# Optimization experiments

Hardware: AMD Instinct MI355X
Metric: run time of the kernel (lower is better)

The kernel has to match this reference:

```python
import jax, jax.numpy as jnp
import numpy as np

B, S, D = 1, 2048, 4096
NH, NKV, HD = 32, 8, 128
N_REP = NH // NKV
NEG = -1e9


def setup_inputs() -> dict:
    key = jax.random.key(0)
    ks = jax.random.split(key, 8)
    x = jax.random.normal(ks[0], (B, S, D), dtype=jnp.float32)
    # rotary freqs (theta=10000), shape [S, HD//2]
    inv = 1.0 / (10000.0 ** (jnp.arange(0, HD, 2, dtype=jnp.float32) / HD))
    ang = jnp.arange(S, dtype=jnp.float32)[:, None] * inv[None, :]
    freqs_cos, freqs_sin = jnp.cos(ang), jnp.sin(ang)
    # causal mask [1,1,S,S]
    row = jnp.arange(S)[:, None]
    col = jnp.arange(S)[None, :]
    mask = jnp.where(col <= row, 0.0, NEG).astype(jnp.float32)[None, None]
    input_indexes = jnp.arange(S, dtype=jnp.int64)
    cache_k = jnp.zeros((B, S, NKV, HD), dtype=jnp.float32)
    cache_v = jnp.zeros((B, S, NKV, HD), dtype=jnp.float32)
    sc = 0.02
    wq = jax.random.normal(ks[1], (NH * HD, D), dtype=jnp.float32) * sc
    wk = jax.random.normal(ks[2], (NKV * HD, D), dtype=jnp.float32) * sc
    wv = jax.random.normal(ks[3], (NKV * HD, D), dtype=jnp.float32) * sc
    wo = jax.random.normal(ks[4], (NH * HD, D), dtype=jnp.float32).T * sc
    return {"x": x, "freqs_cos": freqs_cos, "freqs_sin": freqs_sin, "mask": mask,
            "input_indexes": input_indexes, "cache_k": cache_k, "cache_v": cache_v,
            "wq": wq, "wk": wk, "wv": wv, "wo": wo}


def _rope(t, cos, sin):
    # t: [B,S,H,HD]; treat last dim as HD//2 complex pairs (even=real, odd=imag)
    tr = t.reshape(*t.shape[:-1], HD // 2, 2)
    xr, xi = tr[..., 0], tr[..., 1]
    c = cos[None, :, None, :]  # [1,S,1,HD//2]
    s = sin[None, :, None, :]
    outr = xr * c - xi * s
    outi = xr * s + xi * c
    return jnp.stack([outr, outi], axis=-1).reshape(t.shape)


def reference(x, freqs_cos, freqs_sin, mask, input_indexes, cache_k, cache_v, wq, wk, wv, wo):
    bsz, seqlen = x.shape[0], x.shape[-2]
    xq = (x @ wq.T).reshape(bsz, seqlen, NH, HD)
    xk = (x @ wk.T).reshape(bsz, seqlen, NKV, HD)
    xv = (x @ wv.T).reshape(bsz, seqlen, NKV, HD)
    xq = _rope(xq, freqs_cos, freqs_sin)
    xk = _rope(xk, freqs_cos, freqs_sin)
    # KV-cache append (index_copy along seq dim)
    cache_k = cache_k.at[:, input_indexes].set(xk)
    cache_v = cache_v.at[:, input_indexes].set(xv)
    # GQA: repeat kv heads
    keys = jnp.repeat(cache_k, N_REP, axis=2)    # [B,S,NH,HD]
    values = jnp.repeat(cache_v, N_REP, axis=2)
    scores = jnp.einsum('bshd,bthd->bhst', xq, keys) / jnp.sqrt(jnp.float32(HD))
    scores = scores + mask
    probs = jax.nn.softmax(scores.astype(jnp.float32), axis=-1).astype(xq.dtype)
    out = jnp.einsum('bhst,bthd->bhsd', probs, values)
    out = out.transpose(0, 2, 1, 3).reshape(bsz, seqlen, -1)
    return (out @ wo.T, cache_k, cache_v)
```

## Files before the change

### kernel.cpp

```cpp
#include <hip/hip_runtime.h>
#include <cstdint>

#define S_LEN 2048
#define D_DIM 4096
#define NH_ 32
#define NKV_ 8
#define HD_ 128
#define GK 4096

typedef unsigned short u16;
typedef __attribute__((ext_vector_type(4))) float f32x4;
typedef __attribute__((ext_vector_type(8))) short bf16x8;
typedef __attribute__((ext_vector_type(4))) short s16x4;

__device__ __forceinline__ short f2bf(float f) {
  union { float f; unsigned int u; } v; v.f = f;
  unsigned int r = v.u + 0x7fffu + ((v.u >> 16) & 1u);
  return (short)(r >> 16);
}

__device__ __forceinline__ void glds16(const void* g, void* l) {
  __builtin_amdgcn_global_load_lds(
      (const __attribute__((address_space(1))) void*)g,
      (__attribute__((address_space(3))) void*)l, 16, 0, 0);
}

__global__ __launch_bounds__(256) void cvt_bf16(const float* __restrict__ src,
                                                u16* __restrict__ dst, int n8) {
  int i = blockIdx.x * 256 + threadIdx.x;
  if (i < n8) {
    float4 a = *(const float4*)&src[(size_t)i * 8];
    float4 b = *(const float4*)&src[(size_t)i * 8 + 4];
    bf16x8 o = { f2bf(a.x), f2bf(a.y), f2bf(a.z), f2bf(a.w),
                 f2bf(b.x), f2bf(b.y), f2bf(b.z), f2bf(b.w) };
    *(bf16x8*)&dst[(size_t)i * 8] = o;
  }
}

template <int MODE>
__global__ __launch_bounds__(512, 2) void gemm8(const u16* __restrict__ Amat,
                                                const u16* __restrict__ W,
                                                float* __restrict__ C,
                                                u16* __restrict__ qbf,
                                                u16* __restrict__ kbf,
                                                u16* __restrict__ vbf,
                                                float* __restrict__ cko,
                                                float* __restrict__ cvo,
                                                const float* __restrict__ fc,
                                                const float* __restrict__ fs,
                                                int N) {
  __shared__ __align__(16) u16 As[2][16384];
  __shared__ __align__(16) u16 Bs[2][16384];
  const int t = threadIdx.x;
  const int lane = t & 63;
  const int wave = t >> 6;
  const int wr = wave >> 2;
  const int wc = wave & 3;
  const int quad = lane >> 4;
  const int L = lane & 15;
  const int bm = blockIdx.y * 256;
  const int bn = blockIdx.x * 256;
  const int dr = lane >> 3;
  const int cb = lane & 7;
  const int cbs = cb ^ dr;
  const int NT = GK / 64;

  auto stageA = [&](int tile) {
    u16* dst = &As[tile & 1][0];
    const int k0 = tile << 6;
#pragma unroll
    for (int c = 0; c < 4; ++c) {
      const int chunk = wave * 4 + c;
      const int row = chunk * 8 + dr;
      glds16(&Amat[(size_t)(bm + row) * GK + k0 + cbs * 8], &dst[chunk * 512]);
    }
  };
  auto stageB = [&](int tile) {
    u16* dst = &Bs[tile & 1][0];
    const int k0 = tile << 6;
#pragma unroll
    for (int c = 0; c < 4; ++c) {
      const int chunk = wave * 4 + c;
      const int row = chunk * 8 + dr;
      glds16(&W[(size_t)(bn + row) * GK + k0 + cbs * 8], &dst[chunk * 512]);
    }
  };

  f32x4 acc[8][4];
#pragma unroll
  for (int i = 0; i < 8; ++i)
#pragma unroll
    for (int j = 0; j < 4; ++j) { f32x4 z = {0.f, 0.f, 0.f, 0.f}; acc[i][j] = z; }

  stageB(0); stageA(0); stageB(1);
  asm volatile("s_waitcnt vmcnt(4)" ::: "memory");
  __builtin_amdgcn_s_barrier();
  __builtin_amdgcn_sched_barrier(0);

  bf16x8 af[4], bw[4];
  const int arow = wr * 128;
  const int brow = wc * 64;

  for (int kt = 0; kt < NT; ++kt) {
    const u16* as = &As[kt & 1][0];
    const u16* bs = &Bs[kt & 1][0];
#pragma unroll
    for (int ph = 0; ph < 4; ++ph) {
      const int mh = ph & 1;
      const int s = ph >> 1;
#pragma unroll
      for (int i = 0; i < 4; ++i)
        af[i] = *(const bf16x8*)&as[(arow + mh * 64 + i * 16 + L) * 64 +
                                     (((s * 4 + quad) ^ (L & 7)) * 8)];
      if (ph == 0 || ph == 2) {
#pragma unroll
        for (int j = 0; j < 4; ++j)
          bw[j] = *(const bf16x8*)&bs[(brow + j * 16 + L) * 64 +
                                       (((s * 4 + quad) ^ (L & 7)) * 8)];
      }
      if (ph == 0 && kt + 1 < NT) stageA(kt + 1);
      if (ph == 3 && kt + 2 < NT) stageB(kt + 2);
      __builtin_amdgcn_s_barrier();
      asm volatile("s_waitcnt lgkmcnt(0)" ::: "memory");
      __builtin_amdgcn_sched_barrier(0);
      __builtin_amdgcn_s_setprio(1);
#pragma unroll
      for (int i = 0; i < 4; ++i)
#pragma unroll
        for (int j = 0; j < 4; ++j)
          acc[mh * 4 + i][j] = __builtin_amdgcn_mfma_f32_16x16x32_bf16(
              af[i], bw[j], acc[mh * 4 + i][j], 0, 0, 0);
      __builtin_amdgcn_s_setprio(0);
      if (ph == 3) {
        if (kt + 2 < NT) asm volatile("s_waitcnt vmcnt(4)" ::: "memory");
        else             asm volatile("s_waitcnt vmcnt(0)" ::: "memory");
      }
      __builtin_amdgcn_s_barrier();
      __builtin_amdgcn_sched_barrier(0);
    }
  }

  if (MODE == 0) {
#pragma unroll
    for (int mi = 0; mi < 8; ++mi) {
      int r0 = bm + wr * 128 + mi * 16 + quad * 4;
#pragma unroll
      for (int ni = 0; ni < 4; ++ni) {
        int c = bn + wc * 64 + ni * 16 + L;
#pragma unroll
        for (int r = 0; r < 4; ++r) C[(size_t)(r0 + r) * N + c] = acc[mi][ni][r];
      }
    }
  } else {
    const float scale = 0.08838834764831845f;
#pragma unroll
    for (int mi = 0; mi < 8; ++mi) {
#pragma unroll
      for (int ni = 0; ni < 4; ++ni) {
        int c = bn + wc * 64 + ni * 16 + L;
#pragma unroll
        for (int r = 0; r < 4; ++r) {
          int srow = bm + wr * 128 + mi * 16 + 4 * quad + r;
          float v = acc[mi][ni][r];
          float partner = __shfl_xor(v, 1);
          if (c < 4096) {
            int p = (c >> 1) & 63;
            float co = fc[srow * 64 + p], si = fs[srow * 64 + p];
            float out = (c & 1) ? partner * si + v * co : v * co - partner * si;
            qbf[(size_t)srow * 4096 + c] = (u16)f2bf(out * scale);
          } else if (c < 5120) {
            int p = (c >> 1) & 63;
            float co = fc[srow * 64 + p], si = fs[srow * 64 + p];
            float out = (c & 1) ? partner * si + v * co : v * co - partner * si;
            int cc = c - 4096;
            cko[(size_t)srow * 1024 + cc] = out;
            kbf[(size_t)srow * 1024 + cc] = (u16)f2bf(out);
          } else {
            int cc = c - 5120;
            cvo[(size_t)srow * 1024 + cc] = v;
            vbf[(size_t)srow * 1024 + cc] = (u16)f2bf(v);
          }
        }
      }
    }
  }
}

__global__ __launch_bounds__(512, 2) void attn_bf(const u16* __restrict__ qbf,
                                                  const u16* __restrict__ kbf,
                                                  const u16* __restrict__ vbf,
                                                  u16* __restrict__ ao) {
  __shared__ __align__(16) u16 Ks[64 * 136];
  __shared__ __align__(16) u16 Vt[128 * 64];
  __shared__ __align__(16) u16 Ps[8 * 16 * 72];
  const int t = threadIdx.x;
  const int wave = t >> 6;
  const int lane = t & 63;
  const int Q4 = lane >> 4;
  const int L = lane & 15;
  const int h = blockIdx.y;
  const int qb = 15 - (int)blockIdx.x;
  const int kvh = h >> 2;
  const int qs0 = qb * 128;
  u16* Psw = &Ps[wave * 16 * 72];

  bf16x8 qf[4];
  {
    const u16* qbase = &qbf[(size_t)(qs0 + 16 * wave + L) * D_DIM + h * HD_ + 8 * Q4];
#pragma unroll
    for (int s = 0; s < 4; ++s) qf[s] = *(const bf16x8*)&qbase[32 * s];
  }

  f32x4 o[8];
#pragma unroll
  for (int jd = 0; jd < 8; ++jd) { f32x4 z = {0.f, 0.f, 0.f, 0.f}; o[jd] = z; }
  float mold[4] = {-1e30f, -1e30f, -1e30f, -1e30f};
  float lst[4] = {0.f, 0.f, 0.f, 0.f};

  const int NKT = 2 * qb + 2;
  for (int kt = 0; kt < NKT; ++kt) {
    __syncthreads();
    const u16* kb = &kbf[(size_t)(kt * 64) * (NKV_ * HD_) + kvh * HD_];
    const u16* vb = &vbf[(size_t)(kt * 64) * (NKV_ * HD_) + kvh * HD_];
#pragma unroll
    for (int p = 0; p < 2; ++p) {
      int u = t + 512 * p;
      int r = u >> 4, c8 = u & 15;
      *(bf16x8*)&Ks[r * 136 + c8 * 8] =
          *(const bf16x8*)&kb[(size_t)r * (NKV_ * HD_) + c8 * 8];
    }
#pragma unroll
    for (int p = 0; p < 2; ++p) {
      int u = t + 512 * p;
      int d = u & 127, bb = u >> 7;
      const u16* vsrc = &vb[(size_t)(bb * 8) * (NKV_ * HD_) + d];
      short vv[8];
#pragma unroll
      for (int j = 0; j < 8; ++j) vv[j] = (short)vsrc[(size_t)j * (NKV_ * HD_)];
      bf16x8 pk = { vv[0], vv[1], vv[2], vv[3], vv[4], vv[5], vv[6], vv[7] };
      *(bf16x8*)&Vt[d * 64 + ((bb + d) & 7) * 8] = pk;
    }
    __syncthreads();

    f32x4 sa[4];
#pragma unroll
    for (int jn = 0; jn < 4; ++jn) { f32x4 z = {0.f, 0.f, 0.f, 0.f}; sa[jn] = z; }
#pragma unroll
    for (int s = 0; s < 4; ++s) {
#pragma unroll
      for (int jn = 0; jn < 4; ++jn) {
        bf16x8 kf = *(const bf16x8*)&Ks[(16 * jn + L) * 136 + 32 * s + 8 * Q4];
        sa[jn] = __builtin_amdgcn_mfma_f32_16x16x32_bf16(qf[s], kf, sa[jn], 0, 0, 0);
      }
    }

    const int gq0 = qs0 + 16 * wave + 4 * Q4;
    const int gk0 = kt * 64 + L;
    float rmax[4];
#pragma unroll
    for (int r = 0; r < 4; ++r) {
#pragma unroll
      for (int jn = 0; jn < 4; ++jn)
        if (gk0 + 16 * jn > gq0 + r) sa[jn][r] = -1e30f;
      rmax[r] = fmaxf(fmaxf(sa[0][r], sa[1][r]), fmaxf(sa[2][r], sa[3][r]));
    }
#pragma unroll
    for (int m = 1; m < 16; m <<= 1) {
#pragma unroll
      for (int r = 0; r < 4; ++r) rmax[r] = fmaxf(rmax[r], __shfl_xor(rmax[r], m));
    }
    float p_[4][4], rsum[4], alpha[4];
#pragma unroll
    for (int r = 0; r < 4; ++r) {
      float mnew = fmaxf(mold[r], rmax[r]);
      alpha[r] = __expf(mold[r] - mnew);
#pragma unroll
      for (int jn = 0; jn < 4; ++jn) p_[jn][r] = __expf(sa[jn][r] - mnew);
      rsum[r] = (p_[0][r] + p_[1][r]) + (p_[2][r] + p_[3][r]);
      mold[r] = mnew;
    }
#pragma unroll
    for (int m = 1; m < 16; m <<= 1) {
#pragma unroll
      for (int r = 0; r < 4; ++r) rsum[r] += __shfl_xor(rsum[r], m);
    }
#pragma unroll
    for (int r = 0; r < 4; ++r) lst[r] = lst[r] * alpha[r] + rsum[r];
#pragma unroll
    for (int jd = 0; jd < 8; ++jd)
#pragma unroll
      for (int r = 0; r < 4; ++r) o[jd][r] *= alpha[r];

#pragma unroll
    for (int r = 0; r < 4; ++r)
#pragma unroll
      for (int jn = 0; jn < 4; ++jn)
        Psw[(4 * Q4 + r) * 72 + 16 * jn + L] = (u16)f2bf(p_[jn][r]);
    asm volatile("s_waitcnt lgkmcnt(0)" ::: "memory");

#pragma unroll
    for (int s2 = 0; s2 < 2; ++s2) {
      bf16x8 pa = *(const bf16x8*)&Psw[L * 72 + 32 * s2 + 8 * Q4];
#pragma unroll
      for (int jd = 0; jd < 8; ++jd) {
        bf16x8 vf = *(const bf16x8*)&Vt[(16 * jd + L) * 64 + ((4 * s2 + Q4 + L) & 7) * 8];
        o[jd] = __builtin_amdgcn_mfma_f32_16x16x32_bf16(pa, vf, o[jd], 0, 0, 0);
      }
    }
  }

  float inv[4];
#pragma unroll
  for (int r = 0; r < 4; ++r) inv[r] = 1.0f / lst[r];
#pragma unroll
  for (int r = 0; r < 4; ++r) {
    u16* dst = &ao[(size_t)(qs0 + 16 * wave + 4 * Q4 + r) * D_DIM + h * HD_ + L];
#pragma unroll
    for (int jd = 0; jd < 8; ++jd) dst[16 * jd] = (u16)f2bf(o[jd][r] * inv[r]);
  }
}

#define LDA 40
__global__ __launch_bounds__(256) void gemm_bt(const float* __restrict__ A,
                                               const float* __restrict__ W,
                                               float* __restrict__ C, int N) {
  __shared__ short As[128 * LDA];
  __shared__ short Bs[128 * LDA];
  const int t = threadIdx.x;
  const int lane = t & 63;
  const int wave = t >> 6;
  const int wm = (wave >> 1) * 64;
  const int wn = (wave & 1) * 64;
  const int quad = lane >> 4;
  const int l15 = lane & 15;
  const int bm = blockIdx.y * 128;
  const int bn = blockIdx.x * 128;
  f32x4 acc[4][4];
#pragma unroll
  for (int i = 0; i < 4; ++i)
#pragma unroll
    for (int j = 0; j < 4; ++j) { f32x4 z = {0.f, 0.f, 0.f, 0.f}; acc[i][j] = z; }
  for (int k0 = 0; k0 < GK; k0 += 32) {
    __syncthreads();
#pragma unroll
    for (int p = 0; p < 4; ++p) {
      int idx = p * 256 + t;
      int row = idx >> 3;
      int c4 = (idx & 7) * 4;
      const float4 av = *(const float4*)&A[(size_t)(bm + row) * GK + k0 + c4];
      const float4 wv = *(const float4*)&W[(size_t)(bn + row) * GK + k0 + c4];
      s16x4 a4 = { f2bf(av.x), f2bf(av.y), f2bf(av.z), f2bf(av.w) };
      s16x4 w4 = { f2bf(wv.x), f2bf(wv.y), f2bf(wv.z), f2bf(wv.w) };
      *(s16x4*)&As[row * LDA + c4] = a4;
      *(s16x4*)&Bs[row * LDA + c4] = w4;
    }
    __syncthreads();
    bf16x8 af[4], bfr[4];
#pragma unroll
    for (int i = 0; i < 4; ++i) {
      af[i]  = *(const bf16x8*)&As[(wm + i * 16 + l15) * LDA + quad * 8];
      bfr[i] = *(const bf16x8*)&Bs[(wn + i * 16 + l15) * LDA + quad * 8];
    }
#pragma unroll
    for (int i = 0; i < 4; ++i)
#pragma unroll
      for (int j = 0; j < 4; ++j)
        acc[i][j] = __builtin_amdgcn_mfma_f32_16x16x32_bf16(af[i], bfr[j], acc[i][j], 0, 0, 0);
  }
#pragma unroll
  for (int i = 0; i < 4; ++i) {
    int r0 = bm + wm + i * 16 + quad * 4;
#pragma unroll
    for (int j = 0; j < 4; ++j) {
      int c = bn + wn + j * 16 + l15;
#pragma unroll
      for (int r = 0; r < 4; ++r) C[(size_t)(r0 + r) * N + c] = acc[i][j][r];
    }
  }
}

__global__ __launch_bounds__(256) void rope_kernel(float* __restrict__ xq,
                                                   const float* __restrict__ xk,
                                                   float* __restrict__ cko,
                                                   const float* __restrict__ fc,
                                                   const float* __restrict__ fs) {
  int i = blockIdx.x * 256 + threadIdx.x;
  const int NQP = S_LEN * NH_ * (HD_ / 2);
  if (i < NQP) {
    int s = i >> 11; int rem = i & 2047; int p = rem & 63;
    float c = fc[s * 64 + p], sn = fs[s * 64 + p];
    float2 v = *(const float2*)&xq[(size_t)s * D_DIM + 2 * rem];
    *(float2*)&xq[(size_t)s * D_DIM + 2 * rem] =
        make_float2(v.x * c - v.y * sn, v.x * sn + v.y * c);
  } else {
    int j = i - NQP; int s = j >> 9; int rem = j & 511; int p = rem & 63;
    float c = fc[s * 64 + p], sn = fs[s * 64 + p];
    float2 v = *(const float2*)&xk[(size_t)s * (NKV_ * HD_) + 2 * rem];
    *(float2*)&cko[(size_t)s * (NKV_ * HD_) + 2 * rem] =
        make_float2(v.x * c - v.y * sn, v.x * sn + v.y * c);
  }
}

__global__ __launch_bounds__(256, 3) void attn_mfma(const float* __restrict__ xq,
                                                    const float* __restrict__ ck,
                                                    const float* __restrict__ cv,
                                                    float* __restrict__ outp) {
  __shared__ __align__(16) short Ks[64 * 136];
  __shared__ __align__(16) short Vt[128 * 64];
  __shared__ __align__(16) short Ps[4 * 16 * 72];
  const int t = threadIdx.x;
  const int wave = t >> 6;
  const int lane = t & 63;
  const int Q4 = lane >> 4;
  const int L = lane & 15;
  const int h = blockIdx.y;
  const int qb = 31 - (int)blockIdx.x;
  const int kvh = h >> 2;
  const int qs0 = qb * 64;
  const float scale = 0.08838834764831845f;
  short* Psw = &Ps[wave * 16 * 72];
  bf16x8 qf[4];
  {
    const float* qbase = &xq[(size_t)(qs0 + 16 * wave + L) * D_DIM + h * HD_ + 8 * Q4];
#pragma unroll
    for (int s = 0; s < 4; ++s) {
      float4 a = *(const float4*)&qbase[32 * s];
      float4 b = *(const float4*)&qbase[32 * s + 4];
      bf16x8 q8 = { f2bf(a.x * scale), f2bf(a.y * scale), f2bf(a.z * scale), f2bf(a.w * scale),
                    f2bf(b.x * scale), f2bf(b.y * scale), f2bf(b.z * scale), f2bf(b.w * scale) };
      qf[s] = q8;
    }
  }
  f32x4 o[8];
#pragma unroll
  for (int jd = 0; jd < 8; ++jd) { f32x4 z = {0.f, 0.f, 0.f, 0.f}; o[jd] = z; }
  float mold[4] = {-1e30f, -1e30f, -1e30f, -1e30f};
  float lst[4] = {0.f, 0.f, 0.f, 0.f};
  for (int kt = 0; kt <= qb; ++kt) {
    __syncthreads();
    const float* ckb = &ck[(size_t)(kt * 64) * (NKV_ * HD_) + kvh * HD_];
    const float* cvb = &cv[(size_t)(kt * 64) * (NKV_ * HD_) + kvh * HD_];
#pragma unroll
    for (int p = 0; p < 8; ++p) {
      int i = t + 256 * p;
      int r = i >> 5, c4 = (i & 31) * 4;
      float4 v = *(const float4*)&ckb[(size_t)r * (NKV_ * HD_) + c4];
      s16x4 k4 = { f2bf(v.x), f2bf(v.y), f2bf(v.z), f2bf(v.w) };
      *(s16x4*)&Ks[r * 136 + c4] = k4;
    }
#pragma unroll
    for (int p = 0; p < 4; ++p) {
      int u = t + 256 * p;
      int d = u & 127, bb = u >> 7;
      float vv[8];
#pragma unroll
      for (int j = 0; j < 8; ++j) vv[j] = cvb[(size_t)(bb * 8 + j) * (NKV_ * HD_) + d];
      bf16x8 pk = { f2bf(vv[0]), f2bf(vv[1]), f2bf(vv[2]), f2bf(vv[3]),
                    f2bf(vv[4]), f2bf(vv[5]), f2bf(vv[6]), f2bf(vv[7]) };
      *(bf16x8*)&Vt[d * 64 + ((bb + d) & 7) * 8] = pk;
    }
    __syncthreads();
    f32x4 sa[4];
#pragma unroll
    for (int jn = 0; jn < 4; ++jn) { f32x4 z = {0.f, 0.f, 0.f, 0.f}; sa[jn] = z; }
#pragma unroll
    for (int s = 0; s < 4; ++s) {
#pragma unroll
      for (int jn = 0; jn < 4; ++jn) {
        bf16x8 kf = *(const bf16x8*)&Ks[(16 * jn + L) * 136 + 32 * s + 8 * Q4];
        sa[jn] = __builtin_amdgcn_mfma_f32_16x16x32_bf16(qf[s], kf, sa[jn], 0, 0, 0);
      }
    }
    const int gq0 = qs0 + 16 * wave + 4 * Q4;
    const int gk0 = kt * 64 + L;
    float rmax[4];
#pragma unroll
    for (int r = 0; r < 4; ++r) {
#pragma unroll
      for (int jn = 0; jn < 4; ++jn)
        if (gk0 + 16 * jn > gq0 + r) sa[jn][r] = -1e30f;
      rmax[r] = fmaxf(fmaxf(sa[0][r], sa[1][r]), fmaxf(sa[2][r], sa[3][r]));
    }
#pragma unroll
    for (int m = 1; m < 16; m <<= 1) {
#pragma unroll
      for (int r = 0; r < 4; ++r) rmax[r] = fmaxf(rmax[r], __shfl_xor(rmax[r], m));
    }
    float p_[4][4], rsum[4], alpha[4];
#pragma unroll
    for (int r = 0; r < 4; ++r) {
      float mnew = fmaxf(mold[r], rmax[r]);
      alpha[r] = __expf(mold[r] - mnew);
#pragma unroll
      for (int jn = 0; jn < 4; ++jn) p_[jn][r] = __expf(sa[jn][r] - mnew);
      rsum[r] = (p_[0][r] + p_[1][r]) + (p_[2][r] + p_[3][r]);
      mold[r] = mnew;
    }
#pragma unroll
    for (int m = 1; m < 16; m <<= 1) {
#pragma unroll
      for (int r = 0; r < 4; ++r) rsum[r] += __shfl_xor(rsum[r], m);
    }
#pragma unroll
    for (int r = 0; r < 4; ++r) lst[r] = lst[r] * alpha[r] + rsum[r];
#pragma unroll
    for (int jd = 0; jd < 8; ++jd)
#pragma unroll
      for (int r = 0; r < 4; ++r) o[jd][r] *= alpha[r];
#pragma unroll
    for (int r = 0; r < 4; ++r)
#pragma unroll
      for (int jn = 0; jn < 4; ++jn)
        Psw[(4 * Q4 + r) * 72 + 16 * jn + L] = f2bf(p_[jn][r]);
    asm volatile("s_waitcnt lgkmcnt(0)" ::: "memory");
#pragma unroll
    for (int s2 = 0; s2 < 2; ++s2) {
      bf16x8 pa = *(const bf16x8*)&Psw[L * 72 + 32 * s2 + 8 * Q4];
#pragma unroll
      for (int jd = 0; jd < 8; ++jd) {
        bf16x8 vf = *(const bf16x8*)&Vt[(16 * jd + L) * 64 + ((4 * s2 + Q4 + L) & 7) * 8];
        o[jd] = __builtin_amdgcn_mfma_f32_16x16x32_bf16(pa, vf, o[jd], 0, 0, 0);
      }
    }
  }
  float inv[4];
#pragma unroll
  for (int r = 0; r < 4; ++r) inv[r] = 1.0f / lst[r];
#pragma unroll
  for (int r = 0; r < 4; ++r) {
    float* dst = &outp[(size_t)(qs0 + 16 * wave + 4 * Q4 + r) * D_DIM + h * HD_ + L];
#pragma unroll
    for (int jd = 0; jd < 8; ++jd) dst[16 * jd] = o[jd][r] * inv[r];
  }
}

extern "C" void kernel_launch(void* const* d_in, const int* in_sizes, int n_in,
                              void* d_out, int out_size, void* d_ws, size_t ws_size,
                              hipStream_t stream) {
  (void)in_sizes; (void)n_in; (void)out_size;
  const float* x  = (const float*)d_in[0];
  const float* fc = (const float*)d_in[1];
  const float* fs = (const float*)d_in[2];
  const float* wq = (const float*)d_in[7];
  const float* wk = (const float*)d_in[8];
  const float* wv = (const float*)d_in[9];
  const float* wo = (const float*)d_in[10];
  float* outp = (float*)d_out;
  float* ck = outp + (size_t)S_LEN * D_DIM;
  float* cv = ck + (size_t)S_LEN * NKV_ * HD_;

  if (ws_size >= 109051904ull) {
    u16* x_bf = (u16*)d_ws;
    u16* wqkv = x_bf + 8388608;
    u16* q_bf = wqkv + 25165824;
    u16* k_bf = q_bf + 8388608;
    u16* v_bf = k_bf + 2097152;
    u16* ao_bf = v_bf + 2097152;
    u16* wo_bf = wqkv;

    cvt_bf16<<<4096, 256, 0, stream>>>(x, x_bf, 1048576);
    cvt_bf16<<<8192, 256, 0, stream>>>(wq, wqkv, 2097152);
    cvt_bf16<<<2048, 256, 0, stream>>>(wk, wqkv + 16777216, 524288);
    cvt_bf16<<<2048, 256, 0, stream>>>(wv, wqkv + 20971520, 524288);
    gemm8<1><<<dim3(24, 8), 512, 0, stream>>>(x_bf, wqkv, nullptr, q_bf,
                                              k_bf, v_bf, ck, cv, fc, fs, 6144);
    cvt_bf16<<<8192, 256, 0, stream>>>(wo, wo_bf, 2097152);
    attn_bf<<<dim3(16, 32), 512, 0, stream>>>(q_bf, k_bf, v_bf, ao_bf);
    gemm8<0><<<dim3(16, 8), 512, 0, stream>>>(ao_bf, wo_bf, outp, nullptr,
                                              nullptr, nullptr, nullptr,
                                              nullptr, fc, fs, 4096);
  } else {
    float* xq = (float*)d_ws;
    float* xk = xq + (size_t)S_LEN * D_DIM;
    dim3 blk(256);
    gemm_bt<<<dim3(32, 16), blk, 0, stream>>>(x, wq, xq, 4096);
    gemm_bt<<<dim3(8, 16),  blk, 0, stream>>>(x, wk, xk, 1024);
    gemm_bt<<<dim3(8, 16),  blk, 0, stream>>>(x, wv, cv, 1024);
    rope_kernel<<<20480, 256, 0, stream>>>(xq, xk, ck, fc, fs);
    attn_mfma<<<dim3(32, 32), 512 / 2, 0, stream>>>(xq, ck, cv, xq);
    gemm_bt<<<dim3(32, 16), blk, 0, stream>>>(xq, wo, outp, 4096);
  }
}
```

Measured before the change: 646.1 us.

## Narrow QKV GEMM tiles and split-K the output projection with atomics

```diff
diff --git a/kernel.cpp b/kernel.cpp
--- a/kernel.cpp
+++ b/kernel.cpp
@@ -37,7 +37,7 @@
   }
 }
 
-template <int MODE>
+template <int MODE, int NI, int ATOMIC>
 __global__ __launch_bounds__(512, 2) void gemm8(const u16* __restrict__ Amat,
                                                 const u16* __restrict__ W,
                                                 float* __restrict__ C,
@@ -48,9 +48,9 @@
                                                 float* __restrict__ cvo,
                                                 const float* __restrict__ fc,
                                                 const float* __restrict__ fs,
-                                                int N) {
+                                                int N, int ktPer) {
   __shared__ __align__(16) u16 As[2][16384];
-  __shared__ __align__(16) u16 Bs[2][16384];
+  __shared__ __align__(16) u16 Bs[2][NI * 4096];
   const int t = threadIdx.x;
   const int lane = t & 63;
   const int wave = t >> 6;
@@ -59,11 +59,12 @@
   const int quad = lane >> 4;
   const int L = lane & 15;
   const int bm = blockIdx.y * 256;
-  const int bn = blockIdx.x * 256;
+  const int bn = blockIdx.x * (NI * 64);
   const int dr = lane >> 3;
   const int cb = lane & 7;
   const int cbs = cb ^ dr;
-  const int NT = GK / 64;
+  const int kt0 = blockIdx.z * ktPer;
+  const int ktN = kt0 + ktPer;
 
   auto stageA = [&](int tile) {
     u16* dst = &As[tile & 1][0];
@@ -79,29 +80,30 @@
     u16* dst = &Bs[tile & 1][0];
     const int k0 = tile << 6;
 #pragma unroll
-    for (int c = 0; c < 4; ++c) {
-      const int chunk = wave * 4 + c;
+    for (int c = 0; c < NI; ++c) {
+      const int chunk = wave * NI + c;
       const int row = chunk * 8 + dr;
       glds16(&W[(size_t)(bn + row) * GK + k0 + cbs * 8], &dst[chunk * 512]);
     }
   };
 
-  f32x4 acc[8][4];
+  f32x4 acc[8][NI];
 #pragma unroll
   for (int i = 0; i < 8; ++i)
 #pragma unroll
-    for (int j = 0; j < 4; ++j) { f32x4 z = {0.f, 0.f, 0.f, 0.f}; acc[i][j] = z; }
-
-  stageB(0); stageA(0); stageB(1);
-  asm volatile("s_waitcnt vmcnt(4)" ::: "memory");
+    for (int j = 0; j < NI; ++j) { f32x4 z = {0.f, 0.f, 0.f, 0.f}; acc[i][j] = z; }
+
+  stageB(kt0); stageA(kt0); stageB(kt0 + 1);
+  if constexpr (NI == 3) asm volatile("s_waitcnt vmcnt(3)" ::: "memory");
+  else                   asm volatile("s_waitcnt vmcnt(4)" ::: "memory");
   __builtin_amdgcn_s_barrier();
   __builtin_amdgcn_sched_barrier(0);
 
-  bf16x8 af[4], bw[4];
+  bf16x8 af[4], bw[NI];
   const int arow = wr * 128;
-  const int brow = wc * 64;
-
-  for (int kt = 0; kt < NT; ++kt) {
+  const int brow = wc * (NI * 16);
+
+  for (int kt = kt0; kt < ktN; ++kt) {
     const u16* as = &As[kt & 1][0];
     const u16* bs = &Bs[kt & 1][0];
 #pragma unroll
@@ -114,12 +116,12 @@
                                      (((s * 4 + quad) ^ (L & 7)) * 8)];
       if (ph == 0 || ph == 2) {
 #pragma unroll
-        for (int j = 0; j < 4; ++j)
+        for (int j = 0; j < NI; ++j)
           bw[j] = *(const bf16x8*)&bs[(brow + j * 16 + L) * 64 +
                                        (((s * 4 + quad) ^ (L & 7)) * 8)];
       }
-      if (ph == 0 && kt + 1 < NT) stageA(kt + 1);
-      if (ph == 3 && kt + 2 < NT) stageB(kt + 2);
+      if (ph == 0 && kt + 1 < ktN) stageA(kt + 1);
+      if (ph == 3 && kt + 2 < ktN) stageB(kt + 2);
       __builtin_amdgcn_s_barrier();
       asm volatile("s_waitcnt lgkmcnt(0)" ::: "memory");
       __builtin_amdgcn_sched_barrier(0);
@@ -127,13 +129,17 @@
 #pragma unroll
       for (int i = 0; i < 4; ++i)
 #pragma unroll
-        for (int j = 0; j < 4; ++j)
+        for (int j = 0; j < NI; ++j)
           acc[mh * 4 + i][j] = __builtin_amdgcn_mfma_f32_16x16x32_bf16(
               af[i], bw[j], acc[mh * 4 + i][j], 0, 0, 0);
       __builtin_amdgcn_s_setprio(0);
       if (ph == 3) {
-        if (kt + 2 < NT) asm volatile("s_waitcnt vmcnt(4)" ::: "memory");
-        else             asm volatile("s_waitcnt vmcnt(0)" ::: "memory");
+        if (kt + 2 < ktN) {
+          if constexpr (NI == 3) asm volatile("s_waitcnt vmcnt(3)" ::: "memory");
+          else                   asm volatile("s_waitcnt vmcnt(4)" ::: "memory");
+        } else {
+          asm volatile("s_waitcnt vmcnt(0)" ::: "memory");
+        }
       }
       __builtin_amdgcn_s_barrier();
       __builtin_amdgcn_sched_barrier(0);
@@ -145,10 +151,13 @@
     for (int mi = 0; mi < 8; ++mi) {
       int r0 = bm + wr * 128 + mi * 16 + quad * 4;
 #pragma unroll
-      for (int ni = 0; ni < 4; ++ni) {
-        int c = bn + wc * 64 + ni * 16 + L;
-#pragma unroll
-        for (int r = 0; r < 4; ++r) C[(size_t)(r0 + r) * N + c] = acc[mi][ni][r];
+      for (int ni = 0; ni < NI; ++ni) {
+        int c = bn + wc * (NI * 16) + ni * 16 + L;
+#pragma unroll
+        for (int r = 0; r < 4; ++r) {
+          if (ATOMIC) unsafeAtomicAdd(&C[(size_t)(r0 + r) * N + c], acc[mi][ni][r]);
+          else        C[(size_t)(r0 + r) * N + c] = acc[mi][ni][r];
+        }
       }
     }
   } else {
@@ -156,8 +165,8 @@
 #pragma unroll
     for (int mi = 0; mi < 8; ++mi) {
 #pragma unroll
-      for (int ni = 0; ni < 4; ++ni) {
-        int c = bn + wc * 64 + ni * 16 + L;
+      for (int ni = 0; ni < NI; ++ni) {
+        int c = bn + wc * (NI * 16) + ni * 16 + L;
 #pragma unroll
         for (int r = 0; r < 4; ++r) {
           int srow = bm + wr * 128 + mi * 16 + 4 * quad + r;
@@ -558,17 +567,19 @@
     u16* ao_bf = v_bf + 2097152;
     u16* wo_bf = wqkv;
 
+    hipMemsetAsync(outp, 0, (size_t)S_LEN * D_DIM * sizeof(float), stream);
+
     cvt_bf16<<<4096, 256, 0, stream>>>(x, x_bf, 1048576);
     cvt_bf16<<<8192, 256, 0, stream>>>(wq, wqkv, 2097152);
     cvt_bf16<<<2048, 256, 0, stream>>>(wk, wqkv + 16777216, 524288);
     cvt_bf16<<<2048, 256, 0, stream>>>(wv, wqkv + 20971520, 524288);
-    gemm8<1><<<dim3(24, 8), 512, 0, stream>>>(x_bf, wqkv, nullptr, q_bf,
-                                              k_bf, v_bf, ck, cv, fc, fs, 6144);
+    gemm8<1, 3, 0><<<dim3(32, 8, 1), 512, 0, stream>>>(
+        x_bf, wqkv, nullptr, q_bf, k_bf, v_bf, ck, cv, fc, fs, 6144, 64);
     cvt_bf16<<<8192, 256, 0, stream>>>(wo, wo_bf, 2097152);
     attn_bf<<<dim3(16, 32), 512, 0, stream>>>(q_bf, k_bf, v_bf, ao_bf);
-    gemm8<0><<<dim3(16, 8), 512, 0, stream>>>(ao_bf, wo_bf, outp, nullptr,
-                                              nullptr, nullptr, nullptr,
-                                              nullptr, fc, fs, 4096);
+    gemm8<0, 4, 1><<<dim3(16, 8, 2), 512, 0, stream>>>(
+        ao_bf, wo_bf, outp, nullptr, nullptr, nullptr, nullptr, nullptr,
+        fc, fs, 4096, 32);
   } else {
     float* xq = (float*)d_ws;
     float* xk = xq + (size_t)S_LEN * D_DIM;
```

Result: faster. 631.1 us (-2.3%).
